# Optimization experiments

Measured on AMD Instinct MI355X. Metric: run time of the kernel, lower is better.

The kernel has to match this reference:

```python
import jax, jax.numpy as jnp
import numpy as np

N, T, V, C, H = 16, 512, 33, 3, 64
EPS = 1e-5
CONNECTIONS = [(0,1),(1,2),(2,3),(3,7),(0,4),(4,5),(5,6),(6,8),(9,10),(11,12),(11,13),(13,15),(12,14),(14,16),(15,17),(15,19),(15,21),(17,19),(16,18),(16,20),(16,22),(18,20),(11,23),(12,24),(23,24),(23,25),(25,27),(24,26),(26,28),(27,29),(27,31),(29,31),(28,30),(28,32)]


def _adjacency():
    A = np.zeros((V, V), dtype=np.float32)
    for i, j in CONNECTIONS:
        A[i, j] = 1.0
        A[j, i] = 1.0
    A = A + np.eye(V, dtype=np.float32)
    return jnp.asarray(A / A.sum(axis=1, keepdims=True))  # D^{-1} A row-normalization


def setup_inputs() -> dict:
    key = jax.random.key(0)
    ks = iter(jax.random.split(key, 80))
    def nrm(shape, s=0.05):
        return jax.random.normal(next(ks), shape, jnp.float32) * s
    d = {"x": jax.random.normal(next(ks), (N, T, V, C), jnp.float32), "A": _adjacency()}
    def bn(prefix, shape):
        d[prefix + "g"] = 1.0 + nrm(shape, 0.1)
        d[prefix + "b"] = nrm(shape, 0.1)
        d[prefix + "m"] = jnp.zeros(shape, jnp.float32)
        d[prefix + "v"] = jnp.ones(shape, jnp.float32)
    bn("dbn_", (C * V,))
    d["b1_gw"] = nrm((H, C)); d["b1_gb"] = nrm((H,))
    bn("b1_bn1", (H,)); d["b1_tw"] = nrm((H, H, 9)); d["b1_tb"] = nrm((H,)); bn("b1_bn2", (H,))
    d["m_gw"] = nrm((3, H, H)); d["m_gb"] = nrm((3, H))
    bn("m_bn1", (3, H)); d["m_tw"] = nrm((3, H, H, 9)); d["m_tb"] = nrm((3, H)); bn("m_bn2", (3, H))
    d["b5_gw"] = nrm((C, H)); d["b5_gb"] = nrm((C,))
    bn("b5_bn1", (C,)); d["b5_tw"] = nrm((C, C, 9)); d["b5_tb"] = nrm((C,)); bn("b5_bn2", (C,))
    return d


def _bn2d(y, g, b, m, v):
    sh = (1, -1, 1, 1)
    return (y - m.reshape(sh)) * (g.reshape(sh) * jax.lax.rsqrt(v.reshape(sh) + EPS)) + b.reshape(sh)


def _block(y, A, gw, gb, g1, b1, m1, v1, tw, tb, g2, b2, m2, v2, residual):
    res = y if residual else 0.0
    # GraphConv: 1x1 conv (K=1 partition) then joint aggregation with normalized adjacency
    z = jnp.einsum('nctv,oc->notv', y, gw) + gb.reshape(1, -1, 1, 1)
    z = jnp.einsum('nctv,vw->nctw', z, A)
    # TCN: BN -> ReLU -> 9x1 temporal conv (pad 4) -> BN (dropout identity in eval)
    z = jax.nn.relu(_bn2d(z, g1, b1, m1, v1))
    z = jax.lax.conv_general_dilated(z, tw[..., None], (1, 1), [(4, 4), (0, 0)],
                                     dimension_numbers=('NCHW', 'OIHW', 'NCHW')) + tb.reshape(1, -1, 1, 1)
    z = _bn2d(z, g2, b2, m2, v2)
    return jax.nn.relu(z + res)


def _forward(x, A, dbn_g, dbn_b, dbn_m, dbn_v, b1_gw, b1_gb, b1_bn1g, b1_bn1b, b1_bn1m, b1_bn1v, b1_tw, b1_tb, b1_bn2g, b1_bn2b, b1_bn2m, b1_bn2v, m_gw, m_gb, m_bn1g, m_bn1b, m_bn1m, m_bn1v, m_tw, m_tb, m_bn2g, m_bn2b, m_bn2m, m_bn2v, b5_gw, b5_gb, b5_bn1g, b5_bn1b, b5_bn1m, b5_bn1v, b5_tw, b5_tb, b5_bn2g, b5_bn2b, b5_bn2m, b5_bn2v):
    xc = jnp.transpose(x, (0, 3, 1, 2))  # N,C,T,V
    # data_bn: raw view of NCTV contiguous buffer as (N, C*V, T), matching torch .view
    xr = xc.reshape(N, C * V, T)
    xr = (xr - dbn_m[:, None]) * (dbn_g[:, None] * jax.lax.rsqrt(dbn_v[:, None] + EPS)) + dbn_b[:, None]
    y = xr.reshape(N, C, T, V)
    y = _block(y, A, b1_gw, b1_gb, b1_bn1g, b1_bn1b, b1_bn1m, b1_bn1v, b1_tw, b1_tb, b1_bn2g, b1_bn2b, b1_bn2m, b1_bn2v, False)
    for i in range(3):
        y = _block(y, A, m_gw[i], m_gb[i], m_bn1g[i], m_bn1b[i], m_bn1m[i], m_bn1v[i], m_tw[i], m_tb[i], m_bn2g[i], m_bn2b[i], m_bn2m[i], m_bn2v[i], True)
    y = _block(y, A, b5_gw, b5_gb, b5_bn1g, b5_bn1b, b5_bn1m, b5_bn1v, b5_tw, b5_tb, b5_bn2g, b5_bn2b, b5_bn2m, b5_bn2v, False)
    return jnp.transpose(xc + y, (0, 2, 3, 1))  # N,T,V,C


def reference(x, A, dbn_g, dbn_b, dbn_m, dbn_v, b1_gw, b1_gb, b1_bn1g, b1_bn1b, b1_bn1m, b1_bn1v, b1_tw, b1_tb, b1_bn2g, b1_bn2b, b1_bn2m, b1_bn2v, m_gw, m_gb, m_bn1g, m_bn1b, m_bn1m, m_bn1v, m_tw, m_tb, m_bn2g, m_bn2b, m_bn2m, m_bn2v, b5_gw, b5_gb, b5_bn1g, b5_bn1b, b5_bn1m, b5_bn1v, b5_tw, b5_tb, b5_bn2g, b5_bn2b, b5_bn2m, b5_bn2v):
    return _forward(x, A, dbn_g, dbn_b, dbn_m, dbn_v, b1_gw, b1_gb, b1_bn1g, b1_bn1b, b1_bn1m, b1_bn1v, b1_tw, b1_tb, b1_bn2g, b1_bn2b, b1_bn2m, b1_bn2v, m_gw, m_gb, m_bn1g, m_bn1b, m_bn1m, m_bn1v, m_tw, m_tb, m_bn2g, m_bn2b, m_bn2m, m_bn2v, b5_gw, b5_gb, b5_bn1g, b5_bn1b, b5_bn1m, b5_bn1v, b5_tw, b5_tb, b5_bn2g, b5_bn2b, b5_bn2m, b5_bn2v)
```

## Files before the change

### kernel.cpp

```cpp
#include <hip/hip_runtime.h>
#include <hip/hip_bf16.h>


constexpr int N_ = 16, T_ = 512, V_ = 33, C_ = 3, H_ = 64;
constexpr float EPS_ = 1e-5f;

typedef __attribute__((ext_vector_type(8))) short short8;
typedef __attribute__((ext_vector_type(4))) float f32x4;

__device__ inline unsigned short f2bf(float f) {
    union { __hip_bfloat16 h; unsigned short u; } cv;
    cv.h = __float2bfloat16(f);
    return cv.u;
}
__device__ inline float bf2f(unsigned short u) {
    union { unsigned short u; __hip_bfloat16 h; } cv;
    cv.u = u;
    return __bfloat162float(cv.h);
}

__global__ __launch_bounds__(256) void k_databn(
    const float* __restrict__ x, float* __restrict__ out,
    const float* __restrict__ g, const float* __restrict__ b,
    const float* __restrict__ m, const float* __restrict__ vv)
{
    int idx = blockIdx.x * 256 + threadIdx.x;
    if (idx >= N_ * T_ * V_ * C_) return;
    int c = idx % C_;
    int rem = idx / C_;
    int v = rem % V_;
    int t = (rem / V_) % T_;
    int j = c * V_ + ((t * V_ + v) >> 9);
    float s = g[j] * rsqrtf(vv[j] + EPS_);
    out[idx] = (x[idx] - m[j]) * s + b[j];
}

__global__ __launch_bounds__(256) void k_prep(
    const float* __restrict__ b1_tw, const float* __restrict__ m_tw,
    const float* __restrict__ b1_gw, const float* __restrict__ m_gw,
    const float* __restrict__ Adj,
    unsigned short* __restrict__ wT_bf, unsigned short* __restrict__ gw_bf,
    unsigned short* __restrict__ ATbf, float* __restrict__ colsum,
    float* __restrict__ gwT_b1)
{
    int idx = blockIdx.x * 256 + threadIdx.x;
    if (idx < 147456) {
        int s = idx / 36864, r = idx % 36864;
        int k = r / 4096, o = (r % 4096) / 64, i = r % 64;
        const float* src = (s == 0) ? b1_tw : (m_tw + (size_t)(s - 1) * 36864);
        wT_bf[idx] = f2bf(src[(o * 64 + i) * 9 + k]);
    } else if (idx < 147456 + 12288) {
        int r = idx - 147456;
        gw_bf[r] = f2bf(m_gw[r]);
    } else if (idx < 147456 + 12288 + 3456) {
        int r = idx - 159744;
        int w = r / 72, vv = r % 72;
        ATbf[r] = (w < 33 && vv < 33) ? f2bf(Adj[vv * 33 + w]) : (unsigned short)0;
    } else if (idx < 147456 + 12288 + 3456 + 48) {
        int w = idx - 163200;
        float s = 0.f;
        if (w < 33)
            for (int vv = 0; vv < 33; ++vv) s += Adj[vv * 33 + w];
        colsum[w] = s;
    } else if (idx < 147456 + 12288 + 3456 + 48 + 192) {
        int r = idx - 163248;
        int c = r / 64, o = r % 64;
        gwT_b1[r] = b1_gw[o * 3 + c];
    }
}

__global__ __launch_bounds__(256) void k_stageA_b1(
    const float* __restrict__ in,
    unsigned short* __restrict__ out,
    const float* __restrict__ Adj,
    const float* __restrict__ gwT,
    const float* __restrict__ gb,
    const float* __restrict__ g1, const float* __restrict__ b1,
    const float* __restrict__ m1, const float* __restrict__ v1)
{
    __shared__ float sy[V_ * 4];
    __shared__ float su[V_ * 68];
    __shared__ float sA[V_ * V_];
    __shared__ float sgwT[3 * 64];

    int nt = blockIdx.x;
    int tid = threadIdx.x;
    const float* src = in + (size_t)nt * (V_ * 3);
    for (int idx = tid; idx < V_ * 3; idx += 256)
        sy[(idx / 3) * 4 + (idx % 3)] = src[idx];
    for (int idx = tid; idx < V_ * V_; idx += 256) sA[idx] = Adj[idx];
    for (int idx = tid; idx < 3 * 64; idx += 256) sgwT[idx] = gwT[idx];
    __syncthreads();

    for (int idx = tid; idx < V_ * 16; idx += 256) {
        int v = idx >> 4, oq = idx & 15, o4 = oq * 4;
        float a0 = gb[o4], a1 = gb[o4 + 1], a2 = gb[o4 + 2], a3 = gb[o4 + 3];
#pragma unroll
        for (int c = 0; c < 3; ++c) {
            float yv = sy[v * 4 + c];
            const float4 w4 = *reinterpret_cast<const float4*>(&sgwT[c * 64 + o4]);
            a0 = fmaf(yv, w4.x, a0); a1 = fmaf(yv, w4.y, a1);
            a2 = fmaf(yv, w4.z, a2); a3 = fmaf(yv, w4.w, a3);
        }
        *reinterpret_cast<float4*>(&su[v * 68 + o4]) = make_float4(a0, a1, a2, a3);
    }
    __syncthreads();

    for (int idx = tid; idx < V_ * 16; idx += 256) {
        int w = idx >> 4, oq = idx & 15, o4 = oq * 4;
        float a0 = 0.f, a1 = 0.f, a2 = 0.f, a3 = 0.f;
        for (int v = 0; v < V_; ++v) {
            float av = sA[v * V_ + w];
            const float4 u4 = *reinterpret_cast<const float4*>(&su[v * 68 + o4]);
            a0 = fmaf(av, u4.x, a0); a1 = fmaf(av, u4.y, a1);
            a2 = fmaf(av, u4.z, a2); a3 = fmaf(av, u4.w, a3);
        }
        float acc[4] = {a0, a1, a2, a3};
        unsigned short r4[4];
#pragma unroll
        for (int j = 0; j < 4; ++j) {
            int o = o4 + j;
            float s = g1[o] * rsqrtf(v1[o] + EPS_);
            float t = b1[o] - m1[o] * s;
            r4[j] = f2bf(fmaxf(fmaf(acc[j], s, t), 0.f));
        }
        *reinterpret_cast<ushort4*>(&out[(size_t)nt * (V_ * 64) + w * 64 + o4]) =
            *reinterpret_cast<ushort4*>(r4);
    }
}

__global__ __launch_bounds__(256) void k_stageA_mfma(
    const unsigned short* __restrict__ in,
    unsigned short* __restrict__ out,
    const unsigned short* __restrict__ ATbf,
    const float* __restrict__ colsum,
    const unsigned short* __restrict__ gwbf,
    const float* __restrict__ gb,
    const float* __restrict__ g1, const float* __restrict__ b1,
    const float* __restrict__ m1, const float* __restrict__ v1)
{
    __shared__ unsigned short Ys[4 * 48 * 72];
    __shared__ unsigned short UT[64 * 72];
    __shared__ float cs[48];

    int nt0 = blockIdx.x * 4;
    int tid = threadIdx.x;
    int wv = tid >> 6, lane = tid & 63;
    int l15 = lane & 15, lg = lane >> 4;
    int o = wv * 16 + l15;

    short8 atf[3][2];
#pragma unroll
    for (int mf = 0; mf < 3; ++mf)
#pragma unroll
        for (int kk = 0; kk < 2; ++kk)
            atf[mf][kk] = *reinterpret_cast<const short8*>(
                ATbf + (16 * mf + l15) * 72 + kk * 32 + lg * 8);
    short8 gwf[2];
#pragma unroll
    for (int kk = 0; kk < 2; ++kk)
        gwf[kk] = *reinterpret_cast<const short8*>(gwbf + o * 64 + kk * 32 + lg * 8);

    float gbl = gb[o];
    float s1 = g1[o] * rsqrtf(v1[o] + EPS_);
    float c1 = b1[o] - m1[o] * s1;

    for (int idx = tid; idx < 1056; idx += 256) {
        int j = idx / 264, r = idx % 264;
        int v = r >> 3, cc = r & 7;
        *reinterpret_cast<short8*>(&Ys[(j * 48 + v) * 72 + cc * 8]) =
            *reinterpret_cast<const short8*>(in + ((size_t)(nt0 + j) * V_ + v) * 64 + cc * 8);
    }
    for (int idx = tid; idx < 540; idx += 256) {
        int j = idx / 135, r = idx % 135;
        int v = 33 + r / 9, cc = r % 9;
        short8 z = {};
        *reinterpret_cast<short8*>(&Ys[(j * 48 + v) * 72 + cc * 8]) = z;
    }
    for (int idx = tid; idx < 128; idx += 256) {
        int oo = idx >> 1, cc = idx & 1;
        short8 z = {};
        *reinterpret_cast<short8*>(&UT[oo * 72 + 48 + cc * 8]) = z;
    }
    if (tid < 48) cs[tid] = colsum[tid];
    __syncthreads();

    for (int j = 0; j < 4; ++j) {
#pragma unroll
        for (int mf = 0; mf < 3; ++mf) {
            f32x4 au = {};
#pragma unroll
            for (int kk = 0; kk < 2; ++kk) {
                short8 a = *reinterpret_cast<const short8*>(
                    &Ys[(j * 48 + 16 * mf + l15) * 72 + kk * 32 + lg * 8]);
                au = __builtin_amdgcn_mfma_f32_16x16x32_bf16(a, gwf[kk], au, 0, 0, 0);
            }
            unsigned short pk[4];
            pk[0] = f2bf(au[0]); pk[1] = f2bf(au[1]);
            pk[2] = f2bf(au[2]); pk[3] = f2bf(au[3]);
            *reinterpret_cast<ushort4*>(&UT[o * 72 + 16 * mf + lg * 4]) =
                *reinterpret_cast<ushort4*>(pk);
        }
        __syncthreads();
        short8 bu[2];
#pragma unroll
        for (int kk = 0; kk < 2; ++kk)
            bu[kk] = *reinterpret_cast<const short8*>(&UT[o * 72 + kk * 32 + lg * 8]);
#pragma unroll
        for (int mf2 = 0; mf2 < 3; ++mf2) {
            f32x4 az = {};
#pragma unroll
            for (int kk = 0; kk < 2; ++kk)
                az = __builtin_amdgcn_mfma_f32_16x16x32_bf16(atf[mf2][kk], bu[kk], az, 0, 0, 0);
#pragma unroll
            for (int r = 0; r < 4; ++r) {
                int w = 16 * mf2 + lg * 4 + r;
                if (w < 33) {
                    float val = az[r] + gbl * cs[w];
                    float y = fmaxf(val * s1 + c1, 0.f);
                    out[((size_t)(nt0 + j) * V_ + w) * 64 + o] = f2bf(y);
                }
            }
        }
        __syncthreads();
    }
}

template <bool RES>
__global__ __launch_bounds__(256) void k_stageB_mfma(
    const unsigned short* __restrict__ z,
    unsigned short* __restrict__ out,
    const unsigned short* __restrict__ wbf,
    const float* __restrict__ tb,
    const float* __restrict__ g2, const float* __restrict__ b2,
    const float* __restrict__ m2, const float* __restrict__ vv2)
{
    __shared__ unsigned short sa[2][72 * 64];

    int bx = blockIdx.x, v = blockIdx.y, n = blockIdx.z;
    int base_t0 = bx * 256;
    int tid = threadIdx.x;
    int wv = tid >> 6, lane = tid & 63;
    int l15 = lane & 15, lg = lane >> 4;
    int o = wv * 16 + l15;

    short8 bw[18];
#pragma unroll
    for (int k = 0; k < 9; ++k)
#pragma unroll
        for (int c = 0; c < 2; ++c)
            bw[k * 2 + c] = *reinterpret_cast<const short8*>(
                wbf + ((k * 64 + o) * 64) + c * 32 + lg * 8);

    float s2 = g2[o] * rsqrtf(vv2[o] + EPS_);
    float c2 = (tb[o] - m2[o]) * s2 + b2[o];

    short8 stg[3];

#define LOADJ(jj)                                                             \
    {                                                                         \
        int t0l = base_t0 + (jj) * 64;                                        \
        _Pragma("unroll")                                                     \
        for (int it = 0; it < 3; ++it) {                                      \
            int idx = tid + it * 256;                                         \
            if (idx < 576) {                                                  \
                int r = idx >> 3;                                             \
                int tg = t0l - 4 + r;                                         \
                short8 val = {};                                              \
                if (tg >= 0 && tg < T_)                                       \
                    val = *reinterpret_cast<const short8*>(                   \
                        z + ((size_t)(n * T_ + tg) * V_ + v) * 64 +           \
                        (idx & 7) * 8);                                       \
                stg[it] = val;                                                \
            }                                                                 \
        }                                                                     \
    }

#define WRITEJ(pp)                                                            \
    {                                                                         \
        _Pragma("unroll")                                                     \
        for (int it = 0; it < 3; ++it) {                                      \
            int idx = tid + it * 256;                                         \
            if (idx < 576) {                                                  \
                int r = idx >> 3, cc = idx & 7;                               \
                int slot = cc ^ (r & 7);                                      \
                *reinterpret_cast<short8*>(                                   \
                    reinterpret_cast<char*>(&sa[pp][0]) + r * 128 +           \
                    slot * 16) = stg[it];                                     \
            }                                                                 \
        }                                                                     \
    }

    LOADJ(0);
    WRITEJ(0);
    __syncthreads();

    int p = 0;
    for (int j = 0; j < 4; ++j) {
        if (j < 3) LOADJ(j + 1);

        int t0 = base_t0 + j * 64;

        unsigned short res[16];
        if (RES) {
#pragma unroll
            for (int f = 0; f < 4; ++f)
#pragma unroll
                for (int r = 0; r < 4; ++r) {
                    int t = t0 + f * 16 + lg * 4 + r;
                    res[f * 4 + r] =
                        out[((size_t)(n * T_ + t) * V_ + v) * 64 + o];
                }
        }

        f32x4 acc[4] = {};
        for (int k = 0; k < 9; ++k) {
#pragma unroll
            for (int c = 0; c < 2; ++c) {
                short8 b = bw[k * 2 + c];
#pragma unroll
                for (int f = 0; f < 4; ++f) {
                    int r = f * 16 + l15 + k;
                    int slot = (c * 4 + lg) ^ (r & 7);
                    short8 a = *reinterpret_cast<const short8*>(
                        reinterpret_cast<const char*>(&sa[p][0]) + r * 128 + slot * 16);
                    acc[f] = __builtin_amdgcn_mfma_f32_16x16x32_bf16(a, b, acc[f], 0, 0, 0);
                }
            }
        }

#pragma unroll
        for (int f = 0; f < 4; ++f) {
#pragma unroll
            for (int r = 0; r < 4; ++r) {
                int t = t0 + f * 16 + lg * 4 + r;
                size_t addr = ((size_t)(n * T_ + t) * V_ + v) * 64 + o;
                float zz = acc[f][r] * s2 + c2;
                if (RES) zz += bf2f(res[f * 4 + r]);
                out[addr] = f2bf(fmaxf(zz, 0.f));
            }
        }

        if (j < 3) WRITEJ(p ^ 1);
        __syncthreads();
        p ^= 1;
    }
#undef LOADJ
#undef WRITEJ
}

__global__ __launch_bounds__(256) void k_stageA_b5(
    const unsigned short* __restrict__ in,
    float* __restrict__ out,
    const float* __restrict__ Adj,
    const float* __restrict__ gw,
    const float* __restrict__ gb,
    const float* __restrict__ g1, const float* __restrict__ b1,
    const float* __restrict__ m1, const float* __restrict__ v1)
{
    __shared__ float sy[V_ * 64];
    __shared__ float su[V_ * 4];
    __shared__ float sA[V_ * V_];
    int nt = blockIdx.x;
    int tid = threadIdx.x;
    const unsigned short* src = in + (size_t)nt * (V_ * 64);
    for (int idx = tid; idx < 264; idx += 256) {
        short8 val = *reinterpret_cast<const short8*>(src + idx * 8);
#pragma unroll
        for (int e = 0; e < 8; ++e)
            sy[idx * 8 + e] = bf2f((unsigned short)val[e]);
    }
    for (int idx = tid; idx < V_ * V_; idx += 256) sA[idx] = Adj[idx];
    __syncthreads();
    for (int idx = tid; idx < V_ * 3; idx += 256) {
        int v = idx / 3, o = idx % 3;
        float a = gb[o];
        for (int c = 0; c < 64; ++c) a = fmaf(sy[v * 64 + c], gw[o * 64 + c], a);
        su[v * 4 + o] = a;
    }
    __syncthreads();
    for (int idx = tid; idx < V_ * 3; idx += 256) {
        int w = idx / 3, o = idx % 3;
        float a = 0.f;
        for (int vv = 0; vv < V_; ++vv) a = fmaf(su[vv * 4 + o], sA[vv * V_ + w], a);
        float s = g1[o] * rsqrtf(v1[o] + EPS_);
        float zz = (a - m1[o]) * s + b1[o];
        out[(size_t)nt * (V_ * 3) + w * 3 + o] = fmaxf(zz, 0.f);
    }
}

__global__ __launch_bounds__(256) void k_stageB_b5(
    const float* __restrict__ z5,
    const float* __restrict__ x,
    float* __restrict__ out,
    const float* __restrict__ tw,
    const float* __restrict__ tb,
    const float* __restrict__ g2, const float* __restrict__ b2,
    const float* __restrict__ m2, const float* __restrict__ v2)
{
    int idx = blockIdx.x * 256 + threadIdx.x;
    if (idx >= N_ * T_ * V_) return;
    int v = idx % V_;
    int t = (idx / V_) % T_;
    int n = idx / (V_ * T_);
    float acc0 = tb[0], acc1 = tb[1], acc2 = tb[2];
    for (int k = 0; k < 9; ++k) {
        int tg = t + k - 4;
        if (tg < 0 || tg >= T_) continue;
        const float* zp = &z5[((size_t)(n * T_ + tg) * V_ + v) * 3];
        float zi0 = zp[0], zi1 = zp[1], zi2 = zp[2];
        acc0 = fmaf(tw[0 * 9 + k], zi0, acc0);
        acc0 = fmaf(tw[1 * 9 + k], zi1, acc0);
        acc0 = fmaf(tw[2 * 9 + k], zi2, acc0);
        acc1 = fmaf(tw[3 * 9 + k], zi0, acc1);
        acc1 = fmaf(tw[4 * 9 + k], zi1, acc1);
        acc1 = fmaf(tw[5 * 9 + k], zi2, acc1);
        acc2 = fmaf(tw[6 * 9 + k], zi0, acc2);
        acc2 = fmaf(tw[7 * 9 + k], zi1, acc2);
        acc2 = fmaf(tw[8 * 9 + k], zi2, acc2);
    }
    size_t base = (size_t)idx * 3;
    float a[3] = {acc0, acc1, acc2};
#pragma unroll
    for (int oo = 0; oo < 3; ++oo) {
        float s = g2[oo] * rsqrtf(v2[oo] + EPS_);
        float zz = (a[oo] - m2[oo]) * s + b2[oo];
        out[base + oo] = x[base + oo] + fmaxf(zz, 0.f);
    }
}

extern "C" void kernel_launch(void* const* d_in, const int* in_sizes, int n_in,
                              void* d_out, int out_size, void* d_ws, size_t ws_size,
                              hipStream_t stream) {
    int a = 0;
    const float* x      = (const float*)d_in[a++];
    const float* Adj    = (const float*)d_in[a++];
    const float* dbn_g  = (const float*)d_in[a++];
    const float* dbn_b  = (const float*)d_in[a++];
    const float* dbn_m  = (const float*)d_in[a++];
    const float* dbn_v  = (const float*)d_in[a++];
    const float* b1_gw  = (const float*)d_in[a++];
    const float* b1_gb  = (const float*)d_in[a++];
    const float* b1_bn1g = (const float*)d_in[a++];
    const float* b1_bn1b = (const float*)d_in[a++];
    const float* b1_bn1m = (const float*)d_in[a++];
    const float* b1_bn1v = (const float*)d_in[a++];
    const float* b1_tw  = (const float*)d_in[a++];
    const float* b1_tb  = (const float*)d_in[a++];
    const float* b1_bn2g = (const float*)d_in[a++];
    const float* b1_bn2b = (const float*)d_in[a++];
    const float* b1_bn2m = (const float*)d_in[a++];
    const float* b1_bn2v = (const float*)d_in[a++];
    const float* m_gw   = (const float*)d_in[a++];
    const float* m_gb   = (const float*)d_in[a++];
    const float* m_bn1g = (const float*)d_in[a++];
    const float* m_bn1b = (const float*)d_in[a++];
    const float* m_bn1m = (const float*)d_in[a++];
    const float* m_bn1v = (const float*)d_in[a++];
    const float* m_tw   = (const float*)d_in[a++];
    const float* m_tb   = (const float*)d_in[a++];
    const float* m_bn2g = (const float*)d_in[a++];
    const float* m_bn2b = (const float*)d_in[a++];
    const float* m_bn2m = (const float*)d_in[a++];
    const float* m_bn2v = (const float*)d_in[a++];
    const float* b5_gw  = (const float*)d_in[a++];
    const float* b5_gb  = (const float*)d_in[a++];
    const float* b5_bn1g = (const float*)d_in[a++];
    const float* b5_bn1b = (const float*)d_in[a++];
    const float* b5_bn1m = (const float*)d_in[a++];
    const float* b5_bn1v = (const float*)d_in[a++];
    const float* b5_tw  = (const float*)d_in[a++];
    const float* b5_tb  = (const float*)d_in[a++];
    const float* b5_bn2g = (const float*)d_in[a++];
    const float* b5_bn2b = (const float*)d_in[a++];
    const float* b5_bn2m = (const float*)d_in[a++];
    const float* b5_bn2v = (const float*)d_in[a++];

    char* ws = (char*)d_ws;
    const size_t S_BIG_B  = (size_t)N_ * T_ * V_ * 64 * 2;
    const size_t S_SM_B   = (size_t)N_ * T_ * V_ * 3 * 4;
    unsigned short* B0     = (unsigned short*)(ws);
    unsigned short* B1     = (unsigned short*)(ws + S_BIG_B);
    float*          buf0   = (float*)(ws + 2 * S_BIG_B);
    float*          z5     = (float*)(ws + 2 * S_BIG_B + S_SM_B);
    unsigned short* wT_bf  = (unsigned short*)(ws + 2 * S_BIG_B + 2 * S_SM_B);
    unsigned short* gw_bf  = wT_bf + 147456;
    unsigned short* ATbf   = gw_bf + 12288;
    float*          colsum = (float*)(ATbf + 3456);
    float*          gwT_b1 = colsum + 48;

    k_databn<<<(N_ * T_ * V_ * C_ + 255) / 256, 256, 0, stream>>>(
        x, buf0, dbn_g, dbn_b, dbn_m, dbn_v);
    k_prep<<<(163440 + 255) / 256, 256, 0, stream>>>(
        b1_tw, m_tw, b1_gw, m_gw, Adj, wT_bf, gw_bf, ATbf, colsum, gwT_b1);

    k_stageA_b1<<<N_ * T_, 256, 0, stream>>>(
        buf0, B1, Adj, gwT_b1, b1_gb, b1_bn1g, b1_bn1b, b1_bn1m, b1_bn1v);
    k_stageB_mfma<false><<<dim3(T_ / 256, V_, N_), 256, 0, stream>>>(
        B1, B0, wT_bf, b1_tb, b1_bn2g, b1_bn2b, b1_bn2m, b1_bn2v);

    for (int i = 0; i < 3; ++i) {
        k_stageA_mfma<<<(N_ * T_) / 4, 256, 0, stream>>>(
            B0, B1, ATbf, colsum, gw_bf + i * 4096, m_gb + i * 64,
            m_bn1g + i * 64, m_bn1b + i * 64, m_bn1m + i * 64, m_bn1v + i * 64);
        k_stageB_mfma<true><<<dim3(T_ / 256, V_, N_), 256, 0, stream>>>(
            B1, B0, wT_bf + (1 + i) * 36864, m_tb + i * 64,
            m_bn2g + i * 64, m_bn2b + i * 64, m_bn2m + i * 64, m_bn2v + i * 64);
    }

    k_stageA_b5<<<N_ * T_, 256, 0, stream>>>(
        B0, z5, Adj, b5_gw, b5_gb, b5_bn1g, b5_bn1b, b5_bn1m, b5_bn1v);
    k_stageB_b5<<<(N_ * T_ * V_ + 255) / 256, 256, 0, stream>>>(
        z5, x, (float*)d_out, b5_tw, b5_tb, b5_bn2g, b5_bn2b, b5_bn2m, b5_bn2v);
}
```

Baseline: 292.7 us.

## Fuse data BN into first graph stage and drop LDS staging in stage A

Removes the standalone data batch-norm kernel and applies the per-(c,v) normalization while loading x inside the first graph-conv kernel. This saves one launch and a full intermediate write and read. The MFMA stage-A kernel also loads its A operands straight from global memory into registers instead of staging them through shared memory. That lets it drop both block-wide barriers, since each wave only reads the UT rows it wrote itself. The trade-off is less coalesced, per-lane global loads and reliance on wave-local ordering of shared-memory accesses.

```diff
diff --git a/kernel.cpp b/kernel.cpp
--- a/kernel.cpp
+++ b/kernel.cpp
@@ -17,22 +17,6 @@
     union { unsigned short u; __hip_bfloat16 h; } cv;
     cv.u = u;
     return __bfloat162float(cv.h);
-}
-
-__global__ __launch_bounds__(256) void k_databn(
-    const float* __restrict__ x, float* __restrict__ out,
-    const float* __restrict__ g, const float* __restrict__ b,
-    const float* __restrict__ m, const float* __restrict__ vv)
-{
-    int idx = blockIdx.x * 256 + threadIdx.x;
-    if (idx >= N_ * T_ * V_ * C_) return;
-    int c = idx % C_;
-    int rem = idx / C_;
-    int v = rem % V_;
-    int t = (rem / V_) % T_;
-    int j = c * V_ + ((t * V_ + v) >> 9);
-    float s = g[j] * rsqrtf(vv[j] + EPS_);
-    out[idx] = (x[idx] - m[j]) * s + b[j];
 }
 
 __global__ __launch_bounds__(256) void k_prep(
@@ -70,13 +54,15 @@
 }
 
 __global__ __launch_bounds__(256) void k_stageA_b1(
-    const float* __restrict__ in,
+    const float* __restrict__ x,
     unsigned short* __restrict__ out,
     const float* __restrict__ Adj,
     const float* __restrict__ gwT,
     const float* __restrict__ gb,
     const float* __restrict__ g1, const float* __restrict__ b1,
-    const float* __restrict__ m1, const float* __restrict__ v1)
+    const float* __restrict__ m1, const float* __restrict__ v1,
+    const float* __restrict__ dg, const float* __restrict__ db,
+    const float* __restrict__ dm, const float* __restrict__ dv)
 {
     __shared__ float sy[V_ * 4];
     __shared__ float su[V_ * 68];
@@ -84,10 +70,15 @@
     __shared__ float sgwT[3 * 64];
 
     int nt = blockIdx.x;
+    int t = nt & (T_ - 1);
     int tid = threadIdx.x;
-    const float* src = in + (size_t)nt * (V_ * 3);
-    for (int idx = tid; idx < V_ * 3; idx += 256)
-        sy[(idx / 3) * 4 + (idx % 3)] = src[idx];
+    const float* src = x + (size_t)nt * (V_ * 3);
+    for (int idx = tid; idx < V_ * 3; idx += 256) {
+        int v = idx / 3, c = idx % 3;
+        int jj = c * V_ + ((t * V_ + v) >> 9);
+        float s = dg[jj] * rsqrtf(dv[jj] + EPS_);
+        sy[v * 4 + c] = (src[idx] - dm[jj]) * s + db[jj];
+    }
     for (int idx = tid; idx < V_ * V_; idx += 256) sA[idx] = Adj[idx];
     for (int idx = tid; idx < 3 * 64; idx += 256) sgwT[idx] = gwT[idx];
     __syncthreads();
@@ -121,8 +112,8 @@
         for (int j = 0; j < 4; ++j) {
             int o = o4 + j;
             float s = g1[o] * rsqrtf(v1[o] + EPS_);
-            float t = b1[o] - m1[o] * s;
-            r4[j] = f2bf(fmaxf(fmaf(acc[j], s, t), 0.f));
+            float tt = b1[o] - m1[o] * s;
+            r4[j] = f2bf(fmaxf(fmaf(acc[j], s, tt), 0.f));
         }
         *reinterpret_cast<ushort4*>(&out[(size_t)nt * (V_ * 64) + w * 64 + o4]) =
             *reinterpret_cast<ushort4*>(r4);
@@ -139,7 +130,6 @@
     const float* __restrict__ g1, const float* __restrict__ b1,
     const float* __restrict__ m1, const float* __restrict__ v1)
 {
-    __shared__ unsigned short Ys[4 * 48 * 72];
     __shared__ unsigned short UT[64 * 72];
     __shared__ float cs[48];
 
@@ -165,43 +155,41 @@
     float s1 = g1[o] * rsqrtf(v1[o] + EPS_);
     float c1 = b1[o] - m1[o] * s1;
 
-    for (int idx = tid; idx < 1056; idx += 256) {
-        int j = idx / 264, r = idx % 264;
-        int v = r >> 3, cc = r & 7;
-        *reinterpret_cast<short8*>(&Ys[(j * 48 + v) * 72 + cc * 8]) =
-            *reinterpret_cast<const short8*>(in + ((size_t)(nt0 + j) * V_ + v) * 64 + cc * 8);
-    }
-    for (int idx = tid; idx < 540; idx += 256) {
-        int j = idx / 135, r = idx % 135;
-        int v = 33 + r / 9, cc = r % 9;
-        short8 z = {};
-        *reinterpret_cast<short8*>(&Ys[(j * 48 + v) * 72 + cc * 8]) = z;
-    }
     for (int idx = tid; idx < 128; idx += 256) {
         int oo = idx >> 1, cc = idx & 1;
-        short8 z = {};
-        *reinterpret_cast<short8*>(&UT[oo * 72 + 48 + cc * 8]) = z;
+        short8 zz = {};
+        *reinterpret_cast<short8*>(&UT[oo * 72 + 48 + cc * 8]) = zz;
     }
     if (tid < 48) cs[tid] = colsum[tid];
     __syncthreads();
 
     for (int j = 0; j < 4; ++j) {
+        const unsigned short* src = in + (size_t)(nt0 + j) * (V_ * 64);
+        short8 ag[3][2];
+#pragma unroll
+        for (int mf = 0; mf < 3; ++mf) {
+            int vrow = 16 * mf + l15;
+#pragma unroll
+            for (int kk = 0; kk < 2; ++kk) {
+                short8 a = {};
+                if (vrow < V_)
+                    a = *reinterpret_cast<const short8*>(
+                        src + vrow * 64 + kk * 32 + lg * 8);
+                ag[mf][kk] = a;
+            }
+        }
 #pragma unroll
         for (int mf = 0; mf < 3; ++mf) {
             f32x4 au = {};
 #pragma unroll
-            for (int kk = 0; kk < 2; ++kk) {
-                short8 a = *reinterpret_cast<const short8*>(
-                    &Ys[(j * 48 + 16 * mf + l15) * 72 + kk * 32 + lg * 8]);
-                au = __builtin_amdgcn_mfma_f32_16x16x32_bf16(a, gwf[kk], au, 0, 0, 0);
-            }
+            for (int kk = 0; kk < 2; ++kk)
+                au = __builtin_amdgcn_mfma_f32_16x16x32_bf16(ag[mf][kk], gwf[kk], au, 0, 0, 0);
             unsigned short pk[4];
             pk[0] = f2bf(au[0]); pk[1] = f2bf(au[1]);
             pk[2] = f2bf(au[2]); pk[3] = f2bf(au[3]);
             *reinterpret_cast<ushort4*>(&UT[o * 72 + 16 * mf + lg * 4]) =
                 *reinterpret_cast<ushort4*>(pk);
         }
-        __syncthreads();
         short8 bu[2];
 #pragma unroll
         for (int kk = 0; kk < 2; ++kk)
@@ -222,7 +210,6 @@
                 }
             }
         }
-        __syncthreads();
     }
 }
 
@@ -481,7 +468,6 @@
     const size_t S_SM_B   = (size_t)N_ * T_ * V_ * 3 * 4;
     unsigned short* B0     = (unsigned short*)(ws);
     unsigned short* B1     = (unsigned short*)(ws + S_BIG_B);
-    float*          buf0   = (float*)(ws + 2 * S_BIG_B);
     float*          z5     = (float*)(ws + 2 * S_BIG_B + S_SM_B);
     unsigned short* wT_bf  = (unsigned short*)(ws + 2 * S_BIG_B + 2 * S_SM_B);
     unsigned short* gw_bf  = wT_bf + 147456;
@@ -489,13 +475,12 @@
     float*          colsum = (float*)(ATbf + 3456);
     float*          gwT_b1 = colsum + 48;
 
-    k_databn<<<(N_ * T_ * V_ * C_ + 255) / 256, 256, 0, stream>>>(
-        x, buf0, dbn_g, dbn_b, dbn_m, dbn_v);
     k_prep<<<(163440 + 255) / 256, 256, 0, stream>>>(
         b1_tw, m_tw, b1_gw, m_gw, Adj, wT_bf, gw_bf, ATbf, colsum, gwT_b1);
 
     k_stageA_b1<<<N_ * T_, 256, 0, stream>>>(
-        buf0, B1, Adj, gwT_b1, b1_gb, b1_bn1g, b1_bn1b, b1_bn1m, b1_bn1v);
+        x, B1, Adj, gwT_b1, b1_gb, b1_bn1g, b1_bn1b, b1_bn1m, b1_bn1v,
+        dbn_g, dbn_b, dbn_m, dbn_v);
     k_stageB_mfma<false><<<dim3(T_ / 256, V_, N_), 256, 0, stream>>>(
         B1, B0, wT_bf, b1_tb, b1_bn2g, b1_bn2b, b1_bn2m, b1_bn2v);
 
```

After: 309.3 us. 5.6% more time.
